# Optimization experiments

Hardware: AMD Instinct MI355X
Metric: run time of the kernel (lower is better)

Reference implementation:

```python
import jax, jax.numpy as jnp
import numpy as np

PH, PW = 16, 16  # patch_size


def setup_inputs() -> dict:
    key = jax.random.key(0)
    k1, k2, k3 = jax.random.split(key, 3)
    B, C, H, W = 32, 3, 512, 512
    N, D = 196, 768
    x = jax.random.normal(k1, (B, C, H, W), dtype=jnp.float32)
    centers = jax.random.randint(k2, (B, N, 2), 0, 512, dtype=jnp.int32)
    Wp = jax.random.normal(k3, (PH * PW * C, D), dtype=jnp.float32) * 0.02
    bp = jnp.zeros((D,), dtype=jnp.float32)
    return {"x": x, "centers": centers, "W": Wp, "b": bp}


def reference(x, centers, W, b):
    # x: [B,C,H,Wd], centers: [B,N,2] (h,w), W: [PH*PW*C, D], b: [D]
    B, C, H, Wd = x.shape
    N = centers.shape[1]
    # start indices clipped to valid range (original zero-pads OOB patches;
    # here we clamp so every center yields one in-bounds patch, fixed count)
    sh = jnp.clip(centers[..., 0] - PH // 2, 0, H - PH)
    sw = jnp.clip(centers[..., 1] - PW // 2, 0, Wd - PW)

    def slice_one(img, h0, w0):
        return jax.lax.dynamic_slice(img, (0, h0, w0), (C, PH, PW))

    per_image = jax.vmap(slice_one, in_axes=(None, 0, 0))   # over N patches
    extract = jax.vmap(per_image, in_axes=(0, 0, 0))        # over batch
    patches = extract(x, sh, sw)                             # [B,N,C,PH,PW]
    flat = patches.reshape(B, N, C * PH * PW)                # flatten(start_dim=1) per patch
    return flat @ W + b                                      # [B,N,D]
```

## Files before the change

### kernel.cpp

```cpp
#include <hip/hip_runtime.h>
#include <hip/hip_bf16.h>
#include <stdint.h>

#define PHh 16
#define PWw 16
#define Bn  32
#define Cn  3
#define Hn  512
#define Wn  512
#define Nn  196
#define Dn  768
#define Kn  768
#define Mn  (Bn * Nn)

typedef __attribute__((ext_vector_type(8))) short   short8;
typedef __attribute__((ext_vector_type(4))) float   f32x4;

__global__ void transpose_w(const float* __restrict__ W,
                            __hip_bfloat16* __restrict__ Wt) {
    __shared__ float tile[32][33];
    int d0 = blockIdx.x * 32;
    int k0 = blockIdx.y * 32;
    int lx = threadIdx.x & 31;
    int ly = threadIdx.x >> 5;
#pragma unroll
    for (int i = 0; i < 4; ++i) {
        int kk = ly + i * 8;
        tile[kk][lx] = W[(size_t)(k0 + kk) * Dn + d0 + lx];
    }
    __syncthreads();
#pragma unroll
    for (int i = 0; i < 4; ++i) {
        int dd = ly + i * 8;
        Wt[(size_t)(d0 + dd) * Kn + k0 + lx] = __float2bfloat16(tile[lx][dd]);
    }
}

__device__ __forceinline__ void gload_lds16(const __hip_bfloat16* g,
                                            __hip_bfloat16* l) {
    __builtin_amdgcn_global_load_lds(
        (const __attribute__((address_space(1))) void*)g,
        (__attribute__((address_space(3))) void*)l, 16, 0, 0);
}

__global__ __launch_bounds__(256, 4) void fused_patch_gemm(
    const float* __restrict__ x,
    const int* __restrict__ centers,
    const __hip_bfloat16* __restrict__ Bt,
    const float* __restrict__ bias,
    float* __restrict__ C) {
    __shared__ __hip_bfloat16 As[64 * 32];
    __shared__ __hip_bfloat16 Bs[128 * 32];

    const int bm = blockIdx.x;
    const int bn = blockIdx.y;
    const int tid = threadIdx.x;
    const int w = tid >> 6;
    const int l = tid & 63;
    const int wr = w >> 1;
    const int wc = w & 1;

    const int ml = tid >> 2;
    const int q  = tid & 3;
    const int m  = bm * 64 + ml;
    const int b  = m / Nn;
    const int2 cc = *reinterpret_cast<const int2*>(centers + 2 * m);
    const int sh = min(max(cc.x - PHh / 2, 0), Hn - PHh);
    const int sw = min(max(cc.y - PWw / 2, 0), Wn - PWw);
    const float* xbase = x + ((size_t)(b * Cn) * Hn + sh) * Wn + sw;
    __hip_bfloat16* adst = As + tid * 8;

    const int srow = w * 16 + (l >> 2);
    const int skk  = (l & 3) * 8;
    const __hip_bfloat16* Bg = Bt + (size_t)(bn * 128 + srow) * Kn + skk;

    const int fr = l & 15;
    const int fq = l >> 4;

    f32x4 acc[2][4] = {};

    auto srcAt = [&](int t) -> const float* {
        int k0 = t * 32 + q * 8;
        int c  = k0 >> 8;
        int ph = (k0 >> 4) & 15;
        int pw = k0 & 15;
        return xbase + ((size_t)c * Hn + ph) * Wn + pw;
    };

    const float* s0 = srcAt(0);
    float4 lo = *reinterpret_cast<const float4*>(s0);
    float4 hi = *reinterpret_cast<const float4*>(s0 + 4);

    for (int t = 0; t < Kn / 32; ++t) {
        gload_lds16(Bg,           Bs + w * 512);
        gload_lds16(Bg + 64 * Kn, Bs + 2048 + w * 512);
        Bg += 32;

        __hip_bfloat16 v[8];
        v[0] = __float2bfloat16(lo.x); v[1] = __float2bfloat16(lo.y);
        v[2] = __float2bfloat16(lo.z); v[3] = __float2bfloat16(lo.w);
        v[4] = __float2bfloat16(hi.x); v[5] = __float2bfloat16(hi.y);
        v[6] = __float2bfloat16(hi.z); v[7] = __float2bfloat16(hi.w);
        *reinterpret_cast<short8*>(adst) = *reinterpret_cast<const short8*>(v);

        const float* sn = srcAt(t < Kn / 32 - 1 ? t + 1 : 0);
        float4 nlo = *reinterpret_cast<const float4*>(sn);
        float4 nhi = *reinterpret_cast<const float4*>(sn + 4);

        __syncthreads();

        short8 af[2], bfrag[4];
#pragma unroll
        for (int mm = 0; mm < 2; ++mm)
            af[mm] = *reinterpret_cast<const short8*>(
                &As[(wr * 32 + mm * 16 + fr) * 32 + fq * 8]);
#pragma unroll
        for (int n = 0; n < 4; ++n)
            bfrag[n] = *reinterpret_cast<const short8*>(
                &Bs[(wc * 64 + n * 16 + fr) * 32 + fq * 8]);
#pragma unroll
        for (int mm = 0; mm < 2; ++mm)
#pragma unroll
            for (int n = 0; n < 4; ++n)
                acc[mm][n] = __builtin_amdgcn_mfma_f32_16x16x32_bf16(
                    af[mm], bfrag[n], acc[mm][n], 0, 0, 0);
        __syncthreads();

        lo = nlo; hi = nhi;
    }

#pragma unroll
    for (int n = 0; n < 4; ++n) {
        int col = bn * 128 + wc * 64 + n * 16 + fr;
        float bv = bias[col];
#pragma unroll
        for (int mm = 0; mm < 2; ++mm) {
            int row0 = bm * 64 + wr * 32 + mm * 16 + fq * 4;
#pragma unroll
            for (int j = 0; j < 4; ++j)
                C[(size_t)(row0 + j) * Dn + col] = acc[mm][n][j] + bv;
        }
    }
}

__global__ void naive_patch_embed(const float* __restrict__ x,
                                  const int* __restrict__ centers,
                                  const float* __restrict__ W,
                                  const float* __restrict__ bias,
                                  float* __restrict__ out) {
    int idx = blockIdx.x * blockDim.x + threadIdx.x;
    if (idx >= Mn * Dn) return;
    int m = idx / Dn;
    int d = idx - m * Dn;
    int b = m / Nn;
    int ch = centers[m * 2 + 0];
    int cw = centers[m * 2 + 1];
    int sh = min(max(ch - 8, 0), Hn - PHh);
    int sw = min(max(cw - 8, 0), Wn - PWw);
    float accv = bias[d];
    for (int c = 0; c < Cn; ++c)
        for (int ph = 0; ph < PHh; ++ph) {
            const float* row = x + ((size_t)(b * Cn + c) * Hn + sh + ph) * Wn + sw;
            const float* wr = W + (size_t)(c * 256 + ph * 16) * Dn + d;
#pragma unroll
            for (int pw = 0; pw < PWw; ++pw)
                accv += row[pw] * wr[(size_t)pw * Dn];
        }
    out[idx] = accv;
}

extern "C" void kernel_launch(void* const* d_in, const int* in_sizes, int n_in,
                              void* d_out, int out_size, void* d_ws, size_t ws_size,
                              hipStream_t stream) {
    const float* x       = (const float*)d_in[0];
    const int*   centers = (const int*)d_in[1];
    const float* W       = (const float*)d_in[2];
    const float* bias    = (const float*)d_in[3];
    float*       out     = (float*)d_out;

    const size_t needW = (size_t)Kn * Dn * sizeof(__hip_bfloat16);

    if (ws_size >= needW) {
        __hip_bfloat16* Wt = (__hip_bfloat16*)d_ws;

        dim3 g2(Dn / 32, Kn / 32);
        transpose_w<<<g2, 256, 0, stream>>>(W, Wt);

        dim3 g3(Mn / 64, Dn / 128);
        fused_patch_gemm<<<g3, 256, 0, stream>>>(x, centers, Wt, bias, out);
    } else {
        int g = (Mn * Dn + 255) / 256;
        naive_patch_embed<<<g, 256, 0, stream>>>(x, centers, W, bias, out);
    }
}
```

Before: 165.9 us.

## Double-buffer A and B LDS tiles to overlap loads with MFMA

Gives the fused gather-GEMM kernel ping-pong shared-memory buffers for both the patch (A) and weight (B) tiles. The next tile's A conversion/write and B async global-to-LDS load are issued before the current tile's MFMAs, so only one barrier per iteration remains. This is meant to hide global and LDS latency behind compute. In exchange LDS use per block doubles, which could reduce occupancy, and there is a two-stage register prefetch of A.

```diff
diff --git a/kernel.cpp b/kernel.cpp
--- a/kernel.cpp
+++ b/kernel.cpp
@@ -12,6 +12,7 @@
 #define Dn  768
 #define Kn  768
 #define Mn  (Bn * Nn)
+#define NT  (Kn / 32)
 
 typedef __attribute__((ext_vector_type(8))) short   short8;
 typedef __attribute__((ext_vector_type(4))) float   f32x4;
@@ -49,8 +50,8 @@
     const __hip_bfloat16* __restrict__ Bt,
     const float* __restrict__ bias,
     float* __restrict__ C) {
-    __shared__ __hip_bfloat16 As[64 * 32];
-    __shared__ __hip_bfloat16 Bs[128 * 32];
+    __shared__ __hip_bfloat16 As[2][64 * 32];
+    __shared__ __hip_bfloat16 Bs[2][128 * 32];
 
     const int bm = blockIdx.x;
     const int bn = blockIdx.y;
@@ -68,11 +69,10 @@
     const int sh = min(max(cc.x - PHh / 2, 0), Hn - PHh);
     const int sw = min(max(cc.y - PWw / 2, 0), Wn - PWw);
     const float* xbase = x + ((size_t)(b * Cn) * Hn + sh) * Wn + sw;
-    __hip_bfloat16* adst = As + tid * 8;
 
     const int srow = w * 16 + (l >> 2);
     const int skk  = (l & 3) * 8;
-    const __hip_bfloat16* Bg = Bt + (size_t)(bn * 128 + srow) * Kn + skk;
+    const __hip_bfloat16* Bg0 = Bt + (size_t)(bn * 128 + srow) * Kn + skk;
 
     const int fr = l & 15;
     const int fq = l >> 4;
@@ -86,47 +86,63 @@
         int pw = k0 & 15;
         return xbase + ((size_t)c * Hn + ph) * Wn + pw;
     };
-
-    const float* s0 = srcAt(0);
-    float4 lo = *reinterpret_cast<const float4*>(s0);
-    float4 hi = *reinterpret_cast<const float4*>(s0 + 4);
-
-    for (int t = 0; t < Kn / 32; ++t) {
-        gload_lds16(Bg,           Bs + w * 512);
-        gload_lds16(Bg + 64 * Kn, Bs + 2048 + w * 512);
-        Bg += 32;
-
+    auto stageB = [&](int bi, int t) {
+        const __hip_bfloat16* g = Bg0 + t * 32;
+        gload_lds16(g,           &Bs[bi][w * 512]);
+        gload_lds16(g + 64 * Kn, &Bs[bi][2048 + w * 512]);
+    };
+    auto writeA = [&](int bi, float4 lo, float4 hi) {
         __hip_bfloat16 v[8];
         v[0] = __float2bfloat16(lo.x); v[1] = __float2bfloat16(lo.y);
         v[2] = __float2bfloat16(lo.z); v[3] = __float2bfloat16(lo.w);
         v[4] = __float2bfloat16(hi.x); v[5] = __float2bfloat16(hi.y);
         v[6] = __float2bfloat16(hi.z); v[7] = __float2bfloat16(hi.w);
-        *reinterpret_cast<short8*>(adst) = *reinterpret_cast<const short8*>(v);
-
-        const float* sn = srcAt(t < Kn / 32 - 1 ? t + 1 : 0);
-        float4 nlo = *reinterpret_cast<const float4*>(sn);
-        float4 nhi = *reinterpret_cast<const float4*>(sn + 4);
-
-        __syncthreads();
+        *reinterpret_cast<short8*>(&As[bi][tid * 8]) =
+            *reinterpret_cast<const short8*>(v);
+    };
+
+    stageB(0, 0);
+    {
+        const float* s0 = srcAt(0);
+        float4 lo = *reinterpret_cast<const float4*>(s0);
+        float4 hi = *reinterpret_cast<const float4*>(s0 + 4);
+        writeA(0, lo, hi);
+    }
+    const float* s1 = srcAt(1);
+    float4 plo = *reinterpret_cast<const float4*>(s1);
+    float4 phi = *reinterpret_cast<const float4*>(s1 + 4);
+    __syncthreads();
+
+    int cur = 0;
+    for (int t = 0; t < NT; ++t) {
+        if (t + 1 < NT) {
+            writeA(cur ^ 1, plo, phi);
+            stageB(cur ^ 1, t + 1);
+            if (t + 2 < NT) {
+                const float* sn = srcAt(t + 2);
+                plo = *reinterpret_cast<const float4*>(sn);
+                phi = *reinterpret_cast<const float4*>(sn + 4);
+            }
+        }
 
         short8 af[2], bfrag[4];
 #pragma unroll
         for (int mm = 0; mm < 2; ++mm)
             af[mm] = *reinterpret_cast<const short8*>(
-                &As[(wr * 32 + mm * 16 + fr) * 32 + fq * 8]);
+                &As[cur][(wr * 32 + mm * 16 + fr) * 32 + fq * 8]);
 #pragma unroll
         for (int n = 0; n < 4; ++n)
             bfrag[n] = *reinterpret_cast<const short8*>(
-                &Bs[(wc * 64 + n * 16 + fr) * 32 + fq * 8]);
+                &Bs[cur][(wc * 64 + n * 16 + fr) * 32 + fq * 8]);
 #pragma unroll
         for (int mm = 0; mm < 2; ++mm)
 #pragma unroll
             for (int n = 0; n < 4; ++n)
                 acc[mm][n] = __builtin_amdgcn_mfma_f32_16x16x32_bf16(
                     af[mm], bfrag[n], acc[mm][n], 0, 0, 0);
+
         __syncthreads();
-
-        lo = nlo; hi = nhi;
+        cur ^= 1;
     }
 
 #pragma unroll
```

After: 171.1 us. 3.1% more time.
